# Kernel optimization log

Measured on AMD Instinct MI355X. Metric: run time of the kernel, lower is better.

Reference implementation:

```python
import jax, jax.numpy as jnp
import numpy as np

N = 25000        # nodes
E = 400000       # edges (avg 16 neighbors)
C1 = 8           # output_size (scalar channels into TP)
COUT = 16        # channels_out
LMAX = 2
NB = 8           # number_of_basis
RMAX = 5.0       # max_radius
EMB = 16         # atom embedding dim
NATOM = 10
WNUM = (LMAX + 1) * C1 * COUT                 # per-edge TP weights (parity-shared, k0 paths)
TOTAL_DIM = 2 * COUT * (1 + 3 + 9)            # both parities x ranks 0..2 -> 416


def setup_inputs() -> dict:
    key = jax.random.key(0)
    ks = jax.random.split(key, 12)
    rn = lambda i, shape, s=1.0: jax.random.normal(ks[i], shape, jnp.float32) * s
    pos = rn(0, (N, 3)) * 3.0
    A = jax.random.randint(ks[1], (N,), 0, NATOM)
    batch = jnp.zeros((N,), jnp.int32)                       # single graph
    edge_src = jax.random.randint(ks[2], (E,), 0, N)
    # avoid self-edges (zero-length vectors)
    edge_dst = (edge_src + jax.random.randint(ks[3], (E,), 1, N)) % N
    edge_shifts = jnp.zeros((E, 3), jnp.float32)
    cell = jnp.eye(3, dtype=jnp.float32)[None] * 10.0        # [1,3,3]
    emb_table = rn(4, (NATOM, EMB))
    atom_w1 = rn(5, (EMB, 64), EMB ** -0.5)
    atom_b1 = jnp.zeros((64,), jnp.float32)
    atom_w2 = rn(6, (64, C1), 64 ** -0.5)
    atom_b2 = jnp.zeros((C1,), jnp.float32)
    fc_w1 = rn(7, (NB, 64), NB ** -0.5)
    fc_b1 = jnp.zeros((64,), jnp.float32)
    fc_w2 = rn(8, (64, 64), 64 ** -0.5)
    fc_b2 = jnp.zeros((64,), jnp.float32)
    fc_w3 = rn(9, (64, WNUM), 64 ** -0.5)
    fc_b3 = jnp.zeros((WNUM,), jnp.float32)
    return dict(pos=pos, A=A, batch=batch, edge_src=edge_src, edge_dst=edge_dst,
                edge_shifts=edge_shifts, cell=cell, emb_table=emb_table,
                atom_w1=atom_w1, atom_b1=atom_b1, atom_w2=atom_w2, atom_b2=atom_b2,
                fc_w1=fc_w1, fc_b1=fc_b1, fc_w2=fc_w2, fc_b2=fc_b2, fc_w3=fc_w3, fc_b3=fc_b3)


def reference(pos, A, batch, edge_src, edge_dst, edge_shifts, cell, emb_table,
              atom_w1, atom_b1, atom_w2, atom_b2,
              fc_w1, fc_b1, fc_w2, fc_b2, fc_w3, fc_b3):
    num_edges = edge_src.shape[0]
    num_nodes = pos.shape[0]
    # edge geometry (PBC shift)
    edge_cells = cell[batch[edge_src]]                                   # [E,3,3]
    shift_vecs = jnp.einsum('ni,nij->nj', edge_shifts, edge_cells)
    edge_vec = pos[edge_dst] - pos[edge_src] + shift_vecs                # [E,3]
    edge_length = jnp.sqrt(jnp.sum(edge_vec * edge_vec, axis=1) + 1e-12)
    # per-node scalar features -> gathered to edges
    Ai = jax.nn.silu(emb_table[A] @ atom_w1 + atom_b1) @ atom_w2 + atom_b2  # [N,C1]
    Ai_e = Ai[edge_src]                                                    # [E,C1]
    # edge_rank_powers (normalized): rank-0 scalar 1, rank-1 u, rank-2 u\otimes u
    u = edge_vec / edge_length[:, None]
    # radial basis: e3nn soft_one_hot_linspace (gaussian, cutoff) * sqrt(NB)
    values = jnp.linspace(0.0, RMAX, NB + 2)[1:-1]
    step = RMAX / (NB + 1)
    diff = (edge_length[:, None] - values) / step
    emb = (jnp.exp(-diff * diff) / 1.12) * (NB ** 0.5)                     # [E,NB]
    # radial MLP -> per-edge TP weights
    h = jax.nn.silu(emb @ fc_w1 + fc_b1)
    h = jax.nn.silu(h @ fc_w2 + fc_b2)
    w = (h @ fc_w3 + fc_b3).reshape(num_edges, LMAX + 1, C1, COUT)
    # sparse cartesian O(3) tensor product (k0 paths; only (0,0)x(0,L)->(0,L) nonzero
    # since all x1 L>=1 and parity-1 blocks are zero by construction)
    b0 = jnp.einsum('eco,ec->eo', w[:, 0], Ai_e)                           # [E,COUT]
    b1 = jnp.einsum('eco,ec,ei->eoi', w[:, 1], Ai_e, u)                    # [E,COUT,3]
    b2 = jnp.einsum('eco,ec,ei,ej->eoij', w[:, 2], Ai_e, u, u)             # [E,COUT,3,3]
    feats = jnp.concatenate([b0, b1.reshape(num_edges, -1), b2.reshape(num_edges, -1)], axis=1)
    edge_features = jnp.concatenate([feats, jnp.zeros_like(feats)], axis=1)  # pseudo blocks = 0
    # scatter-sum to destination nodes, normalize by global avg num neighbors
    out = jax.ops.segment_sum(edge_features, edge_dst, num_segments=num_nodes)
    avg_num_neighbors = jnp.maximum(jnp.float32(num_edges) / jnp.float32(num_nodes), 1e-8)
    return out / avg_num_neighbors
```

## Files before the change

### kernel.cpp

```cpp
#include <hip/hip_runtime.h>
#include <math.h>

#define NN 25000
#define NE 400000
#define TD 416
#define TCAP 46080
#define NROWS (TCAP * 10)
#define PLH 64
#define GROWS 32

typedef __attribute__((ext_vector_type(8))) __bf16 bf16x8;
typedef __attribute__((ext_vector_type(4))) _Float16 f16x4;
typedef __attribute__((ext_vector_type(4))) float f32x4;

__device__ __forceinline__ float silu_f(float x) {
    return x * (1.0f / (1.0f + __expf(-x)));
}

__global__ __launch_bounds__(256) void prep_count_k(
    const float* __restrict__ emb_table,
    const float* __restrict__ aw1, const float* __restrict__ ab1,
    const float* __restrict__ aw2, const float* __restrict__ ab2,
    const float* __restrict__ fw1, const float* __restrict__ fb1,
    const float* __restrict__ fw2,
    const float* __restrict__ fw3, const float* __restrict__ fb3,
    __bf16* __restrict__ w1a, __bf16* __restrict__ w2a,
    __bf16* __restrict__ w3ta, float* __restrict__ b3t,
    const int* __restrict__ esrc, const int* __restrict__ edst,
    const int* __restrict__ A,
    int* __restrict__ cnt_dst, int* __restrict__ cnt_t,
    int* __restrict__ rdst, int* __restrict__ rtp) {
    const int tid = threadIdx.x;
    if (blockIdx.x < 64) {
        __shared__ float s_ai[80];
        if (tid < 10) {
            float acc[8];
#pragma unroll
            for (int o = 0; o < 8; ++o) acc[o] = ab2[o];
            for (int j = 0; j < 64; ++j) {
                float h = ab1[j];
#pragma unroll
                for (int i = 0; i < 16; ++i) h += emb_table[tid * 16 + i] * aw1[i * 64 + j];
                h = silu_f(h);
#pragma unroll
                for (int o = 0; o < 8; ++o) acc[o] += h * aw2[j * 8 + o];
            }
#pragma unroll
            for (int o = 0; o < 8; ++o) s_ai[tid * 8 + o] = acc[o];
        }
        __syncthreads();
        for (int i = blockIdx.x * 256 + tid; i < 37344; i += 64 * 256) {
            if (i < 2048) {
                int m = i >> 9, r = i & 511, lane = r >> 3, j = r & 7;
                int k = (lane >> 4) * 8 + j, ch = m * 16 + (lane & 15);
                float v = (k < 8) ? fw1[k * 64 + ch] : ((k == 8) ? fb1[ch] : 0.0f);
                w1a[i] = (__bf16)v;
            } else if (i < 6144) {
                int q = i - 2048;
                int mk = q >> 9, lane = (q >> 3) & 63, j = q & 7;
                int m = mk >> 1, kt = mk & 1;
                int k = kt * 32 + (lane >> 4) * 8 + j, ch = m * 16 + (lane & 15);
                w2a[q] = (__bf16)fw2[k * 64 + ch];
            } else if (i < 36864) {
                int q = i - 6144;
                int tmk = q >> 9, lane = (q >> 3) & 63, j = q & 7;
                int kt = tmk & 1, tm = tmk >> 1;
                int t = tm / 3, m = tm - t * 3;
                int k = kt * 32 + (lane >> 4) * 8 + j, ch = m * 16 + (lane & 15);
                int l = ch >> 4, o = ch & 15;
                float s = 0.f;
#pragma unroll
                for (int c = 0; c < 8; ++c)
                    s += s_ai[t * 8 + c] * fw3[k * 384 + l * 128 + c * 16 + o];
                w3ta[q] = (__bf16)s;
            } else {
                int q2 = i - 36864;
                int t = q2 / 48, ch = q2 - t * 48;
                int l = ch >> 4, o = ch & 15;
                float s = 0.f;
#pragma unroll
                for (int c = 0; c < 8; ++c)
                    s += s_ai[t * 8 + c] * fb3[l * 128 + c * 16 + o];
                b3t[q2] = s;
            }
        }
    } else {
        __shared__ int lcnt[10];
        __shared__ int gbase[10];
        if (tid < 10) lcnt[tid] = 0;
        __syncthreads();
        int e = (blockIdx.x - 64) * 256 + tid;
        int t = 0, lr = 0;
        bool valid = e < NE;
        if (valid) {
            rdst[e] = atomicAdd(&cnt_dst[edst[e]], 1);
            t = A[esrc[e]];
            lr = atomicAdd(&lcnt[t], 1);
        }
        __syncthreads();
        if (tid < 10) gbase[tid] = atomicAdd(&cnt_t[tid], lcnt[tid]);
        __syncthreads();
        if (valid) rtp[e] = (t << 20) | (gbase[t] + lr);
    }
}

__global__ __launch_bounds__(256) void alloc_k(const int* __restrict__ cnt_dst,
                                               int* __restrict__ off_dst,
                                               int* __restrict__ bump) {
    __shared__ int s[256];
    __shared__ int sbase;
    const int tid = threadIdx.x;
    const int idx = blockIdx.x * 256 + tid;
    int c = (idx < NN) ? cnt_dst[idx] : 0;
    s[tid] = c;
    __syncthreads();
    for (int off = 1; off < 256; off <<= 1) {
        int v = (tid >= off) ? s[tid - off] : 0;
        __syncthreads();
        s[tid] += v;
        __syncthreads();
    }
    if (tid == 255) sbase = atomicAdd(bump, s[255]);
    __syncthreads();
    if (idx < NN) off_dst[idx] = sbase + s[tid] - c;
}

__global__ void scatter_k(const int* __restrict__ edst,
                          const int* __restrict__ off_dst,
                          const int* __restrict__ rdst, const int* __restrict__ rtp,
                          int* __restrict__ elist, int* __restrict__ tlist) {
    int e = blockIdx.x * blockDim.x + threadIdx.x;
    if (e >= NE) return;
    int rp = rtp[e];
    int p = (rp >> 20) * TCAP + (rp & 0xFFFFF);
    tlist[p] = e;
    elist[off_dst[edst[e]] + rdst[e]] = p;
}

__global__ __launch_bounds__(64) void edge_k(
    const int* __restrict__ tlist, const int* __restrict__ A,
    const int* __restrict__ esrc, const int* __restrict__ edst,
    const float* __restrict__ pos, const float* __restrict__ shifts,
    const float* __restrict__ cell, const int* __restrict__ batch,
    const __bf16* __restrict__ w1a, const __bf16* __restrict__ w2a,
    const __bf16* __restrict__ w3ta,
    const float* __restrict__ fb2, const float* __restrict__ b3t,
    _Float16* __restrict__ payload) {
    __shared__ __bf16 embuf[64 * 18];
    __shared__ __align__(16) __bf16 zbuf[16];
    __shared__ __bf16 h1buf[16 * 72];
    __shared__ __bf16 h2buf[16 * 72];
    __shared__ float4 ubuf[64];
    const int lane = threadIdx.x;
    const int base = blockIdx.x * 64;
    const int e0 = tlist[base];
    if (e0 < 0) return;
    int t_blk = __builtin_amdgcn_readfirstlane(A[esrc[e0]]);

    int eid = tlist[base + lane];
    if (eid < 0) eid = e0;

    const int src = esrc[eid], dstn = edst[eid];
    const int b = batch[src];
    const float* cb = cell + b * 9;
    const float sh0 = shifts[eid * 3 + 0], sh1 = shifts[eid * 3 + 1], sh2 = shifts[eid * 3 + 2];
    float vx = pos[dstn * 3 + 0] - pos[src * 3 + 0] + sh0 * cb[0] + sh1 * cb[3] + sh2 * cb[6];
    float vy = pos[dstn * 3 + 1] - pos[src * 3 + 1] + sh0 * cb[1] + sh1 * cb[4] + sh2 * cb[7];
    float vz = pos[dstn * 3 + 2] - pos[src * 3 + 2] + sh0 * cb[2] + sh1 * cb[5] + sh2 * cb[8];
    const float len = sqrtf(vx * vx + vy * vy + vz * vz + 1e-12f);
    const float il = 1.0f / len;
    ubuf[lane] = make_float4(vx * il, vy * il, vz * il, 0.f);

    bf16x8 er0;
#pragma unroll
    for (int k = 0; k < 8; ++k) {
        float d = (len - (5.0f * (float)(k + 1) / 9.0f)) * 1.8f;
        er0[k] = (__bf16)(__expf(-d * d) * 2.525381361380528f);
    }
    bf16x8 er1 = {};
    er1[0] = (__bf16)1.0f;
    *(bf16x8*)&embuf[lane * 18 + 0] = er0;
    *(bf16x8*)&embuf[lane * 18 + 8] = er1;
    if (lane < 2) {
        bf16x8 zz = {};
        *(bf16x8*)&zbuf[lane * 8] = zz;
    }

    bf16x8 a1[4], a2[8], a3[6];
#pragma unroll
    for (int m = 0; m < 4; ++m) a1[m] = *(const bf16x8*)(w1a + (m * 64 + lane) * 8);
#pragma unroll
    for (int i = 0; i < 8; ++i) a2[i] = *(const bf16x8*)(w2a + (i * 64 + lane) * 8);
#pragma unroll
    for (int i = 0; i < 6; ++i)
        a3[i] = *(const bf16x8*)(w3ta + ((size_t)(t_blk * 6 + i) * 64 + lane) * 8);
    const int qr = (lane >> 4) * 4;
    const int q8 = (lane >> 4) * 8;
    f32x4 bias2[4], bias3[3];
#pragma unroll
    for (int m = 0; m < 4; ++m) bias2[m] = *(const f32x4*)(fb2 + m * 16 + qr);
#pragma unroll
    for (int m = 0; m < 3; ++m) bias3[m] = *(const f32x4*)(b3t + t_blk * 48 + m * 16 + qr);
    __syncthreads();

    const float SC = (float)NN / (float)NE;
    const int colrow = lane & 15;
#pragma unroll 1
    for (int n = 0; n < 4; ++n) {
        const int erow = n * 16 + colrow;
        const __bf16* bp = (q8 < 16) ? &embuf[erow * 18 + q8] : &zbuf[q8 - 16];
        bf16x8 b1 = *(const bf16x8*)bp;
#pragma unroll
        for (int m = 0; m < 4; ++m) {
            f32x4 c = {0.f, 0.f, 0.f, 0.f};
            c = __builtin_amdgcn_mfma_f32_16x16x32_bf16(a1[m], b1, c, 0, 0, 0);
            __bf16 hp[4];
#pragma unroll
            for (int r = 0; r < 4; ++r) hp[r] = (__bf16)silu_f(c[r]);
            *(uint2*)&h1buf[colrow * 72 + m * 16 + qr] = *(uint2*)hp;
        }
        __syncthreads();
        bf16x8 b20 = *(bf16x8*)&h1buf[colrow * 72 + q8];
        bf16x8 b21 = *(bf16x8*)&h1buf[colrow * 72 + 32 + q8];
#pragma unroll
        for (int m = 0; m < 4; ++m) {
            f32x4 c = bias2[m];
            c = __builtin_amdgcn_mfma_f32_16x16x32_bf16(a2[m * 2 + 0], b20, c, 0, 0, 0);
            c = __builtin_amdgcn_mfma_f32_16x16x32_bf16(a2[m * 2 + 1], b21, c, 0, 0, 0);
            __bf16 hp[4];
#pragma unroll
            for (int r = 0; r < 4; ++r) hp[r] = (__bf16)silu_f(c[r]);
            *(uint2*)&h2buf[colrow * 72 + m * 16 + qr] = *(uint2*)hp;
        }
        __syncthreads();
        bf16x8 b30 = *(bf16x8*)&h2buf[colrow * 72 + q8];
        bf16x8 b31 = *(bf16x8*)&h2buf[colrow * 72 + 32 + q8];
#pragma unroll
        for (int m = 0; m < 3; ++m) {
            f32x4 c = bias3[m];
            c = __builtin_amdgcn_mfma_f32_16x16x32_bf16(a3[m * 2 + 0], b30, c, 0, 0, 0);
            c = __builtin_amdgcn_mfma_f32_16x16x32_bf16(a3[m * 2 + 1], b31, c, 0, 0, 0);
            f16x4 hp;
#pragma unroll
            for (int r = 0; r < 4; ++r) hp[r] = (_Float16)(c[r] * SC);
            *(f16x4*)(payload + (size_t)(base + erow) * PLH + m * 16 + qr) = hp;
        }
        if (lane >= 48) {
            int r = n * 16 + (lane - 48);
            float4 u = ubuf[r];
            _Float16* pr = payload + (size_t)(base + r) * PLH;
            *(uint4*)(pr + 48) = *(uint4*)&u;
            uint4 z4 = make_uint4(0, 0, 0, 0);
            *(uint4*)(pr + 56) = z4;
        }
        __syncthreads();
    }
}

__global__ __launch_bounds__(256) void gather_k(const int* __restrict__ off_dst,
                                                const int* __restrict__ cnt_dst,
                                                const int* __restrict__ elist,
                                                const _Float16* __restrict__ payload,
                                                float* __restrict__ out) {
    __shared__ int spid[GROWS];
    __shared__ __align__(16) _Float16 sp_s[GROWS][72];
    __shared__ float sfac[GROWS][16];
    const int n = blockIdx.x;
    const int tid = threadIdx.x;
    const int lo = off_dst[n];
    const int cnt = cnt_dst[n];
    int voff = 0, foff = 0;
    if (tid < 16) { voff = tid; foff = 0; }
    else if (tid < 64) { int q = tid - 16; voff = 16 + q / 3; foff = 1 + q % 3; }
    else if (tid < 208) { int q = tid - 64; voff = 32 + q / 9; foff = 4 + q % 9; }
    float acc = 0.f;
    for (int p0 = 0; p0 < cnt; p0 += GROWS) {
        const int m = min(GROWS, cnt - p0);
        if (tid < m) spid[tid] = elist[lo + p0 + tid];
        __syncthreads();
        if (tid < m * 8) {
            int r = tid >> 3, q = tid & 7;
            ((uint4*)&sp_s[r][0])[q] = ((const uint4*)(payload + (size_t)spid[r] * PLH))[q];
        }
        __syncthreads();
        for (int idx = tid; idx < m * 16; idx += 256) {
            int r = idx >> 4, f = idx & 15;
            if (f < 13) {
                const float* uf = (const float*)&sp_s[r][48];
                float v;
                if (f == 0) v = 1.0f;
                else if (f < 4) v = uf[f - 1];
                else { int g = f - 4; v = uf[g / 3] * uf[g % 3]; }
                sfac[r][f] = v;
            }
        }
        __syncthreads();
        if (tid < 208)
            for (int r = 0; r < m; ++r)
                acc += (float)sp_s[r][voff] * sfac[r][foff];
        __syncthreads();
    }
    if (tid < 208) {
        out[(size_t)n * TD + tid] = acc;
        out[(size_t)n * TD + 208 + tid] = 0.f;
    }
}

extern "C" void kernel_launch(void* const* d_in, const int* in_sizes, int n_in,
                              void* d_out, int out_size, void* d_ws, size_t ws_size,
                              hipStream_t stream) {
    const float* pos       = (const float*)d_in[0];
    const int*   A         = (const int*)d_in[1];
    const int*   batch     = (const int*)d_in[2];
    const int*   esrc      = (const int*)d_in[3];
    const int*   edst      = (const int*)d_in[4];
    const float* shifts    = (const float*)d_in[5];
    const float* cell      = (const float*)d_in[6];
    const float* emb_table = (const float*)d_in[7];
    const float* aw1       = (const float*)d_in[8];
    const float* ab1       = (const float*)d_in[9];
    const float* aw2       = (const float*)d_in[10];
    const float* ab2       = (const float*)d_in[11];
    const float* fw1       = (const float*)d_in[12];
    const float* fb1       = (const float*)d_in[13];
    const float* fw2       = (const float*)d_in[14];
    const float* fb2       = (const float*)d_in[15];
    const float* fw3       = (const float*)d_in[16];
    const float* fb3       = (const float*)d_in[17];
    float* out = (float*)d_out;

    char* base = (char*)d_ws;
    __bf16* w1a    = (__bf16*)(base + 0);
    __bf16* w2a    = (__bf16*)(base + 4096);
    __bf16* w3ta   = (__bf16*)(base + 12288);
    float*  b3t    = (float*)(base + 73728);
    int* cnt_dst   = (int*)(base + 75648);
    int* cnt_t     = (int*)(base + 175680);
    int* bump      = (int*)(base + 175744);
    int* off_dst   = (int*)(base + 175808);
    int* rdst      = (int*)(base + 275840);
    int* rtp       = (int*)(base + 1875840);
    int* elist     = (int*)(base + 3475840);
    int* tlist     = (int*)(base + 5075840);
    _Float16* payload = (_Float16*)(base + 6919168);

    hipMemsetAsync(cnt_dst, 0, 100160, stream);
    hipMemsetAsync(tlist, 0xFF, NROWS * 4, stream);
    prep_count_k<<<64 + (NE + 255) / 256, 256, 0, stream>>>(
        emb_table, aw1, ab1, aw2, ab2, fw1, fb1, fw2, fw3, fb3,
        w1a, w2a, w3ta, b3t, esrc, edst, A, cnt_dst, cnt_t, rdst, rtp);
    alloc_k<<<(NN + 255) / 256, 256, 0, stream>>>(cnt_dst, off_dst, bump);
    scatter_k<<<(NE + 255) / 256, 256, 0, stream>>>(edst, off_dst, rdst, rtp, elist, tlist);
    edge_k<<<NROWS / 64, 64, 0, stream>>>(tlist, A, esrc, edst, pos, shifts, cell, batch,
                                          w1a, w2a, w3ta, fb2, b3t, payload);
    gather_k<<<NN, 256, 0, stream>>>(off_dst, cnt_dst, elist, payload, out);
}
```

Before: 220.9 us.

## Drop edge-ordering intermediates, shrink type buckets, remove syncs in edge MLP

Per-edge type bucketing now happens inside scatter_k, and destination slots come from an atomic cursor. This removes the rdst/rtp intermediate arrays and their global round trip, and prep_count_k now only counts destinations. Per-type bucket capacity drops from 46080 to 40960, which cuts edge_k blocks and the tlist memset. The radial-MLP loop in edge_k double-buffers its LDS staging and drops the __syncthreads, relying on each block being a single 64-lane wavefront. The trade-offs: per-node edge order is now nondeterministic, and the smaller capacity only holds if each atom type's edge count stays below 40960.

```diff
diff --git a/kernel.cpp b/kernel.cpp
--- a/kernel.cpp
+++ b/kernel.cpp
@@ -4,7 +4,7 @@
 #define NN 25000
 #define NE 400000
 #define TD 416
-#define TCAP 46080
+#define TCAP 40960
 #define NROWS (TCAP * 10)
 #define PLH 64
 #define GROWS 32
@@ -26,10 +26,8 @@
     const float* __restrict__ fw3, const float* __restrict__ fb3,
     __bf16* __restrict__ w1a, __bf16* __restrict__ w2a,
     __bf16* __restrict__ w3ta, float* __restrict__ b3t,
-    const int* __restrict__ esrc, const int* __restrict__ edst,
-    const int* __restrict__ A,
-    int* __restrict__ cnt_dst, int* __restrict__ cnt_t,
-    int* __restrict__ rdst, int* __restrict__ rtp) {
+    const int* __restrict__ edst,
+    int* __restrict__ cnt_dst) {
     const int tid = threadIdx.x;
     if (blockIdx.x < 64) {
         __shared__ float s_ai[80];
@@ -85,27 +83,14 @@
             }
         }
     } else {
-        __shared__ int lcnt[10];
-        __shared__ int gbase[10];
-        if (tid < 10) lcnt[tid] = 0;
-        __syncthreads();
         int e = (blockIdx.x - 64) * 256 + tid;
-        int t = 0, lr = 0;
-        bool valid = e < NE;
-        if (valid) {
-            rdst[e] = atomicAdd(&cnt_dst[edst[e]], 1);
-            t = A[esrc[e]];
-            lr = atomicAdd(&lcnt[t], 1);
-        }
-        __syncthreads();
-        if (tid < 10) gbase[tid] = atomicAdd(&cnt_t[tid], lcnt[tid]);
-        __syncthreads();
-        if (valid) rtp[e] = (t << 20) | (gbase[t] + lr);
+        if (e < NE) atomicAdd(&cnt_dst[edst[e]], 1);
     }
 }
 
 __global__ __launch_bounds__(256) void alloc_k(const int* __restrict__ cnt_dst,
                                                int* __restrict__ off_dst,
+                                               int* __restrict__ cur_dst,
                                                int* __restrict__ bump) {
     __shared__ int s[256];
     __shared__ int sbase;
@@ -122,19 +107,38 @@
     }
     if (tid == 255) sbase = atomicAdd(bump, s[255]);
     __syncthreads();
-    if (idx < NN) off_dst[idx] = sbase + s[tid] - c;
-}
-
-__global__ void scatter_k(const int* __restrict__ edst,
-                          const int* __restrict__ off_dst,
-                          const int* __restrict__ rdst, const int* __restrict__ rtp,
+    if (idx < NN) {
+        int o = sbase + s[tid] - c;
+        off_dst[idx] = o;
+        cur_dst[idx] = o;
+    }
+}
+
+__global__ void scatter_k(const int* __restrict__ esrc, const int* __restrict__ edst,
+                          const int* __restrict__ A,
+                          int* __restrict__ cnt_t, int* __restrict__ cur_dst,
                           int* __restrict__ elist, int* __restrict__ tlist) {
-    int e = blockIdx.x * blockDim.x + threadIdx.x;
-    if (e >= NE) return;
-    int rp = rtp[e];
-    int p = (rp >> 20) * TCAP + (rp & 0xFFFFF);
-    tlist[p] = e;
-    elist[off_dst[edst[e]] + rdst[e]] = p;
+    __shared__ int lcnt[10];
+    __shared__ int gbase[10];
+    int tid = threadIdx.x;
+    if (tid < 10) lcnt[tid] = 0;
+    __syncthreads();
+    int e = blockIdx.x * blockDim.x + tid;
+    int t = 0, lr = 0;
+    bool valid = e < NE;
+    if (valid) {
+        t = A[esrc[e]];
+        lr = atomicAdd(&lcnt[t], 1);
+    }
+    __syncthreads();
+    if (tid < 10) gbase[tid] = atomicAdd(&cnt_t[tid], lcnt[tid]);
+    __syncthreads();
+    if (valid) {
+        int p = t * TCAP + gbase[t] + lr;
+        tlist[p] = e;
+        int slot = atomicAdd(&cur_dst[edst[e]], 1);
+        elist[slot] = p;
+    }
 }
 
 __global__ __launch_bounds__(64) void edge_k(
@@ -148,8 +152,8 @@
     _Float16* __restrict__ payload) {
     __shared__ __bf16 embuf[64 * 18];
     __shared__ __align__(16) __bf16 zbuf[16];
-    __shared__ __bf16 h1buf[16 * 72];
-    __shared__ __bf16 h2buf[16 * 72];
+    __shared__ __bf16 h1buf[2][16 * 72];
+    __shared__ __bf16 h2buf[2][16 * 72];
     __shared__ float4 ubuf[64];
     const int lane = threadIdx.x;
     const int base = blockIdx.x * 64;
@@ -201,12 +205,12 @@
     for (int m = 0; m < 4; ++m) bias2[m] = *(const f32x4*)(fb2 + m * 16 + qr);
 #pragma unroll
     for (int m = 0; m < 3; ++m) bias3[m] = *(const f32x4*)(b3t + t_blk * 48 + m * 16 + qr);
-    __syncthreads();
 
     const float SC = (float)NN / (float)NE;
     const int colrow = lane & 15;
-#pragma unroll 1
+#pragma unroll
     for (int n = 0; n < 4; ++n) {
+        const int np = n & 1;
         const int erow = n * 16 + colrow;
         const __bf16* bp = (q8 < 16) ? &embuf[erow * 18 + q8] : &zbuf[q8 - 16];
         bf16x8 b1 = *(const bf16x8*)bp;
@@ -217,11 +221,10 @@
             __bf16 hp[4];
 #pragma unroll
             for (int r = 0; r < 4; ++r) hp[r] = (__bf16)silu_f(c[r]);
-            *(uint2*)&h1buf[colrow * 72 + m * 16 + qr] = *(uint2*)hp;
-        }
-        __syncthreads();
-        bf16x8 b20 = *(bf16x8*)&h1buf[colrow * 72 + q8];
-        bf16x8 b21 = *(bf16x8*)&h1buf[colrow * 72 + 32 + q8];
+            *(uint2*)&h1buf[np][colrow * 72 + m * 16 + qr] = *(uint2*)hp;
+        }
+        bf16x8 b20 = *(bf16x8*)&h1buf[np][colrow * 72 + q8];
+        bf16x8 b21 = *(bf16x8*)&h1buf[np][colrow * 72 + 32 + q8];
 #pragma unroll
         for (int m = 0; m < 4; ++m) {
             f32x4 c = bias2[m];
@@ -230,11 +233,10 @@
             __bf16 hp[4];
 #pragma unroll
             for (int r = 0; r < 4; ++r) hp[r] = (__bf16)silu_f(c[r]);
-            *(uint2*)&h2buf[colrow * 72 + m * 16 + qr] = *(uint2*)hp;
-        }
-        __syncthreads();
-        bf16x8 b30 = *(bf16x8*)&h2buf[colrow * 72 + q8];
-        bf16x8 b31 = *(bf16x8*)&h2buf[colrow * 72 + 32 + q8];
+            *(uint2*)&h2buf[np][colrow * 72 + m * 16 + qr] = *(uint2*)hp;
+        }
+        bf16x8 b30 = *(bf16x8*)&h2buf[np][colrow * 72 + q8];
+        bf16x8 b31 = *(bf16x8*)&h2buf[np][colrow * 72 + 32 + q8];
 #pragma unroll
         for (int m = 0; m < 3; ++m) {
             f32x4 c = bias3[m];
@@ -253,7 +255,6 @@
             uint4 z4 = make_uint4(0, 0, 0, 0);
             *(uint4*)(pr + 56) = z4;
         }
-        __syncthreads();
     }
 }
 
@@ -338,19 +339,19 @@
     int* cnt_t     = (int*)(base + 175680);
     int* bump      = (int*)(base + 175744);
     int* off_dst   = (int*)(base + 175808);
-    int* rdst      = (int*)(base + 275840);
-    int* rtp       = (int*)(base + 1875840);
-    int* elist     = (int*)(base + 3475840);
-    int* tlist     = (int*)(base + 5075840);
-    _Float16* payload = (_Float16*)(base + 6919168);
+    int* cur_dst   = (int*)(base + 275840);
+    int* elist     = (int*)(base + 375872);
+    int* tlist     = (int*)(base + 1975872);
+    _Float16* payload = (_Float16*)(base + 3614336);
 
     hipMemsetAsync(cnt_dst, 0, 100160, stream);
     hipMemsetAsync(tlist, 0xFF, NROWS * 4, stream);
     prep_count_k<<<64 + (NE + 255) / 256, 256, 0, stream>>>(
         emb_table, aw1, ab1, aw2, ab2, fw1, fb1, fw2, fw3, fb3,
-        w1a, w2a, w3ta, b3t, esrc, edst, A, cnt_dst, cnt_t, rdst, rtp);
-    alloc_k<<<(NN + 255) / 256, 256, 0, stream>>>(cnt_dst, off_dst, bump);
-    scatter_k<<<(NE + 255) / 256, 256, 0, stream>>>(edst, off_dst, rdst, rtp, elist, tlist);
+        w1a, w2a, w3ta, b3t, edst, cnt_dst);
+    alloc_k<<<(NN + 255) / 256, 256, 0, stream>>>(cnt_dst, off_dst, cur_dst, bump);
+    scatter_k<<<(NE + 255) / 256, 256, 0, stream>>>(esrc, edst, A, cnt_t, cur_dst,
+                                                    elist, tlist);
     edge_k<<<NROWS / 64, 64, 0, stream>>>(tlist, A, esrc, edst, pos, shifts, cell, batch,
                                           w1a, w2a, w3ta, fb2, b3t, payload);
     gather_k<<<NN, 256, 0, stream>>>(off_dst, cnt_dst, elist, payload, out);
```

Result: slower. 245.3 us (+11.1%).
